# Optimization experiments

Hardware: AMD Instinct MI355X
Metric: run time of the kernel (lower is better)

The kernel has to match this reference:

```python
import jax, jax.numpy as jnp
import numpy as np

N_NODES = 100000
N_EDGES = 1600000
IN_F = 64
HID_F = 64
HID_CH = 32
OUT_F = 16


def setup_inputs() -> dict:
    key = jax.random.key(0)
    ks = jax.random.split(key, 12)
    feat = jax.random.normal(ks[0], (N_NODES, IN_F), dtype=jnp.float32)
    edge_src = jax.random.randint(ks[1], (N_EDGES,), 0, N_NODES, dtype=jnp.int32)
    edge_dst = jax.random.randint(ks[2], (N_EDGES,), 0, N_NODES, dtype=jnp.int32)
    s = 1.414 / np.sqrt(IN_F)
    fc1_w = jax.random.normal(ks[3], (HID_F, IN_F), dtype=jnp.float32) * s
    fc1_b = jnp.zeros((HID_F,), dtype=jnp.float32)
    filt_w = jax.random.normal(ks[4], (HID_F, IN_F), dtype=jnp.float32) * s
    filt_b = jnp.zeros((HID_F,), dtype=jnp.float32)
    att_w1 = jax.random.normal(ks[5], (HID_F, HID_CH), dtype=jnp.float32) * (1.0 / np.sqrt(HID_F))
    att_b1 = jnp.zeros((HID_CH,), dtype=jnp.float32)
    att_w2 = jax.random.normal(ks[6], (HID_CH, 1), dtype=jnp.float32) * (1.0 / np.sqrt(HID_CH))
    fc2_w = jax.random.normal(ks[7], (OUT_F, HID_F), dtype=jnp.float32) * (1.414 / np.sqrt(HID_F))
    fc2_b = jnp.zeros((OUT_F,), dtype=jnp.float32)
    return {
        "feat": feat, "edge_src": edge_src, "edge_dst": edge_dst,
        "fc1_w": fc1_w, "fc1_b": fc1_b, "filt_w": filt_w, "filt_b": filt_b,
        "att_w1": att_w1, "att_b1": att_b1, "att_w2": att_w2,
        "fc2_w": fc2_w, "fc2_b": fc2_b,
    }


def _lp_filter(feat, edge_src, edge_dst, filt_w, filt_b):
    # Low-pass (GCN-style) filter: symmetric-normalized neighborhood aggregation
    # of the linearly transformed features.  x: [N, H]
    x = feat @ filt_w.T + filt_b
    ones = jnp.ones((edge_src.shape[0],), dtype=x.dtype)
    deg_out = jax.ops.segment_sum(ones, edge_src, num_segments=N_NODES)
    deg_in = jax.ops.segment_sum(ones, edge_dst, num_segments=N_NODES)
    inv_sqrt_out = jax.lax.rsqrt(jnp.maximum(deg_out, 1.0))
    inv_sqrt_in = jax.lax.rsqrt(jnp.maximum(deg_in, 1.0))
    # gather-transform-scatter: msg_e = x[src_e] * norm_e  ->  sum at dst
    coef = inv_sqrt_out[edge_src] * inv_sqrt_in[edge_dst]  # [E]
    msg = x[edge_src] * coef[:, None]                       # [E, H]
    return jax.ops.segment_sum(msg, edge_dst, num_segments=N_NODES)  # [N, H]


def _channel_attention(z, att_w1, att_b1, att_w2):
    # z: [N, C, H]; semantic (channel) attention a la HAN
    w = jnp.tanh(z @ att_w1 + att_b1) @ att_w2        # [N, C, 1]
    beta = jax.nn.softmax(w.mean(axis=0), axis=0)     # [C, 1]
    return (beta[None, :, :] * z).sum(axis=1)         # [N, H]


def reference(feat, edge_src, edge_dst, fc1_w, fc1_b, filt_w, filt_b,
              att_w1, att_b1, att_w2, fc2_w, fc2_b):
    h1 = jnp.tanh(feat @ fc1_w.T + fc1_b)                          # MLP branch [N, H]
    h2 = _lp_filter(feat, edge_src, edge_dst, filt_w, filt_b)      # graph branch [N, H]
    z = jnp.stack([h1, h2], axis=1)                                # [N, 2, H]
    fused = _channel_attention(z, att_w1, att_b1, att_w2)          # [N, H]
    return fused @ fc2_w.T + fc2_b                                 # [N, OUT_F]
```

## Files before the change

### kernel.cpp

```cpp
#include <hip/hip_runtime.h>
#include <math.h>

#define N_NODESC 100000
#define N_EDGESC 1600000
#define NBUCK 1563
#define BSLACK 1280
#define SCHUNK 4096
#define NSBLK 391

__device__ __forceinline__ float fast_tanh(float x) {
    float ax = fabsf(x);
    float e = __expf(-2.f * ax);
    float r = (1.f - e) * __builtin_amdgcn_rcpf(1.f + e);
    return copysignf(r, x);
}

__global__ void binit_kernel(int* __restrict__ bcur, int* __restrict__ sbcur) {
    int i = blockIdx.x * blockDim.x + threadIdx.x;
    if (i < NBUCK) { bcur[i] = i * BSLACK; sbcur[i] = i * BSLACK; }
}

__global__ __launch_bounds__(1024) void scatter_dual_kernel(
    const int* __restrict__ src, const int* __restrict__ dst,
    int* __restrict__ bcur, int* __restrict__ sbcur,
    unsigned* __restrict__ bedges, unsigned char* __restrict__ sbytes) {
    __shared__ int histd[NBUCK];
    __shared__ int hists[NBUCK];
    int tid = threadIdx.x;
    int e_beg = blockIdx.x * SCHUNK;
    int e_end = min(e_beg + SCHUNK, N_EDGESC);
    for (int i = tid; i < NBUCK; i += 1024) { histd[i] = 0; hists[i] = 0; }
    __syncthreads();

    int ss[4], dd[4];
    int cnt = 0;
    for (int i = e_beg + tid; i < e_end; i += 1024) {
        ss[cnt] = src[i];
        dd[cnt] = dst[i];
        cnt++;
    }
#pragma unroll
    for (int j = 0; j < 4; j++) {
        if (j < cnt) {
            atomicAdd(&histd[dd[j] >> 6], 1);
            atomicAdd(&hists[ss[j] >> 6], 1);
        }
    }
    __syncthreads();
    for (int i = tid; i < NBUCK; i += 1024) {
        int c = histd[i];
        if (c > 0) histd[i] = atomicAdd(&bcur[i], c);
        int c2 = hists[i];
        if (c2 > 0) hists[i] = atomicAdd(&sbcur[i], c2);
    }
    __syncthreads();
#pragma unroll
    for (int j = 0; j < 4; j++) {
        if (j < cnt) {
            int slot = atomicAdd(&histd[dd[j] >> 6], 1);
            bedges[slot] = (unsigned)ss[j] | ((unsigned)(dd[j] & 63) << 17);
            int slot2 = atomicAdd(&hists[ss[j] >> 6], 1);
            sbytes[slot2] = (unsigned char)(ss[j] & 63);
        }
    }
}

__global__ __launch_bounds__(256) void gemm_kernel(
    const float* __restrict__ feat,
    const float* __restrict__ w1, const float* __restrict__ b1,
    const float* __restrict__ w2, const float* __restrict__ b2,
    const int* __restrict__ sbcur, const unsigned char* __restrict__ sbytes,
    float* __restrict__ h1, float* __restrict__ xs) {
    __shared__ float sf[128 * 68];
    __shared__ int ldeg[128];
    int tid = threadIdx.x;
    int base = blockIdx.x * 128;
    if (tid < 128) ldeg[tid] = 0;
    for (int k = 0; k < 8; k++) {
        int fi = tid + k * 256;
        int node = fi >> 4, f4 = fi & 15;
        float4 v = make_float4(0.f, 0.f, 0.f, 0.f);
        if (base + node < N_NODESC)
            v = ((const float4*)feat)[(size_t)(base + node) * 16 + f4];
        float* d = &sf[node * 68 + f4 * 4];
        d[0] = v.x; d[1] = v.y; d[2] = v.z; d[3] = v.w;
    }
    __syncthreads();

#pragma unroll
    for (int h = 0; h < 2; h++) {
        int sb = blockIdx.x * 2 + h;
        if (sb < NBUCK) {
            int sbeg = sb * BSLACK;
            int sm = sbcur[sb] - sbeg;
            for (int i = tid; i < sm; i += 256)
                atomicAdd(&ldeg[h * 64 + (int)sbytes[sbeg + i]], 1);
        }
    }

    int lane = tid & 63;
    int og = __builtin_amdgcn_readfirstlane(tid >> 6);
    const float* wp1 = w1 + og * 16 * 64;
    const float* wp2 = w2 + og * 16 * 64;

    float a1[2][16], a2[2][16];
#pragma unroll
    for (int o = 0; o < 16; o++) {
        float bb1 = b1[og * 16 + o], bb2 = b2[og * 16 + o];
        a1[0][o] = bb1; a1[1][o] = bb1;
        a2[0][o] = bb2; a2[1][o] = bb2;
    }

    for (int fq = 0; fq < 16; fq++) {
        float4 fv0 = *(const float4*)&sf[lane * 68 + fq * 4];
        float4 fv1 = *(const float4*)&sf[(lane + 64) * 68 + fq * 4];
#pragma unroll
        for (int o = 0; o < 16; o++) {
            float4 wv1 = *(const float4*)&wp1[o * 64 + fq * 4];
            float4 wv2 = *(const float4*)&wp2[o * 64 + fq * 4];
            a1[0][o] += fv0.x * wv1.x + fv0.y * wv1.y + fv0.z * wv1.z + fv0.w * wv1.w;
            a1[1][o] += fv1.x * wv1.x + fv1.y * wv1.y + fv1.z * wv1.z + fv1.w * wv1.w;
            a2[0][o] += fv0.x * wv2.x + fv0.y * wv2.y + fv0.z * wv2.z + fv0.w * wv2.w;
            a2[1][o] += fv1.x * wv2.x + fv1.y * wv2.y + fv1.z * wv2.z + fv1.w * wv2.w;
        }
    }

    __syncthreads();

#pragma unroll
    for (int j = 0; j < 2; j++) {
        int g = base + lane + j * 64;
        if (g >= N_NODESC) continue;
        float is = rsqrtf(fmaxf((float)ldeg[j * 64 + lane], 1.f));
#pragma unroll
        for (int oq = 0; oq < 4; oq++) {
            float4 t, u;
            t.x = fast_tanh(a1[j][oq * 4 + 0]); t.y = fast_tanh(a1[j][oq * 4 + 1]);
            t.z = fast_tanh(a1[j][oq * 4 + 2]); t.w = fast_tanh(a1[j][oq * 4 + 3]);
            u.x = a2[j][oq * 4 + 0] * is;   u.y = a2[j][oq * 4 + 1] * is;
            u.z = a2[j][oq * 4 + 2] * is;   u.w = a2[j][oq * 4 + 3] * is;
            ((float4*)h1)[(size_t)g * 16 + og * 4 + oq] = t;
            ((float4*)xs)[(size_t)g * 16 + og * 4 + oq] = u;
        }
    }
}

__global__ __launch_bounds__(256) void agg4_kernel(const int* __restrict__ bcur,
                                                   const unsigned* __restrict__ bedges,
                                                   const float* __restrict__ xs,
                                                   float* __restrict__ h2) {
    __shared__ unsigned eraw[BSLACK];
    __shared__ unsigned eled[BSLACK];
    __shared__ int loff[65];
    __shared__ int lcnt[64];
    __shared__ int lcur[64];
    int tid = threadIdx.x, lane = tid & 63, wid = tid >> 6;
    int b = blockIdx.x;
    int beg = b * BSLACK;
    int m = bcur[b] - beg;

    if (tid < 64) lcnt[tid] = 0;
    __syncthreads();
    for (int i = tid; i < m; i += 256) {
        unsigned pk = bedges[beg + i];
        eraw[i] = pk;
        atomicAdd(&lcnt[pk >> 17], 1);
    }
    __syncthreads();
    if (wid == 0) {
        int c = lcnt[lane];
        int v = c;
#pragma unroll
        for (int off = 1; off < 64; off <<= 1) {
            int t = __shfl_up(v, off, 64);
            if (lane >= off) v += t;
        }
        loff[lane] = v - c;
        lcur[lane] = v - c;
        if (lane == 63) loff[64] = v;
    }
    __syncthreads();
    for (int i = tid; i < m; i += 256) {
        unsigned pk = eraw[i];
        int pos = atomicAdd(&lcur[pk >> 17], 1);
        eled[pos] = pk & 0x1FFFFu;
    }
    __syncthreads();

    int nbase = b * 64;
#pragma unroll 1
    for (int t = 0; t < 16; t++) {
        int nl = wid * 16 + t;
        int s0 = loff[nl], s1 = loff[nl + 1];
        float acc = 0.f;
        for (int k = s0; k < s1; k += 16) {
            int cnt = s1 - k; if (cnt > 16) cnt = 16;
            unsigned sv = eled[min(k + (lane & 15), s1 - 1)];
            float v[16];
#pragma unroll
            for (int j = 0; j < 16; j++) {
                if (j < cnt) {
                    int sj = __shfl((int)sv, j, 64);
                    v[j] = xs[(size_t)sj * 64 + lane];
                }
            }
#pragma unroll
            for (int j = 0; j < 16; j++)
                if (j < cnt) acc += v[j];
        }
        int g = nbase + nl;
        if (g < N_NODESC) {
            float isq = rsqrtf(fmaxf((float)(s1 - s0), 1.f));
            h2[(size_t)g * 64 + lane] = acc * isq;
        }
    }
}

__global__ __launch_bounds__(256) void att_kernel(const float* __restrict__ h1,
                                                  const float* __restrict__ h2,
                                                  const float* __restrict__ aw1,
                                                  const float* __restrict__ ab1,
                                                  const float* __restrict__ aw2,
                                                  float* __restrict__ wsum) {
    __shared__ float sw1[64 * 32];
    __shared__ float sb1[32];
    __shared__ float sw2[32];
    int tid = threadIdx.x;
    for (int i = tid; i < 64 * 32; i += 256) sw1[i] = aw1[i];
    if (tid < 32) { sb1[tid] = ab1[tid]; sw2[tid] = aw2[tid]; }
    __syncthreads();

    int n = blockIdx.x * 256 + tid;
    float sc[2] = {0.f, 0.f};
    if (n < N_NODESC) {
#pragma unroll
        for (int c = 0; c < 2; c++) {
            const float* row = (c == 0 ? h1 : h2) + (size_t)n * 64;
            float acc[32];
#pragma unroll
            for (int k = 0; k < 32; k++) acc[k] = sb1[k];
            for (int fq = 0; fq < 16; fq++) {
                float4 rv = ((const float4*)row)[fq];
#pragma unroll
                for (int k = 0; k < 32; k++) {
                    acc[k] += rv.x * sw1[(fq * 4 + 0) * 32 + k]
                            + rv.y * sw1[(fq * 4 + 1) * 32 + k]
                            + rv.z * sw1[(fq * 4 + 2) * 32 + k]
                            + rv.w * sw1[(fq * 4 + 3) * 32 + k];
                }
            }
            float s = 0.f;
#pragma unroll
            for (int k = 0; k < 32; k++) s += fast_tanh(acc[k]) * sw2[k];
            sc[c] = s;
        }
    }
#pragma unroll
    for (int off = 32; off; off >>= 1) {
        sc[0] += __shfl_down(sc[0], off, 64);
        sc[1] += __shfl_down(sc[1], off, 64);
    }
    if ((threadIdx.x & 63) == 0) {
        atomicAdd(&wsum[0], sc[0]);
        atomicAdd(&wsum[1], sc[1]);
    }
}

__global__ void beta_kernel(const float* __restrict__ wsum, float* __restrict__ beta) {
    float w0 = wsum[0] / (float)N_NODESC, w1 = wsum[1] / (float)N_NODESC;
    float m = fmaxf(w0, w1);
    float e0 = expf(w0 - m), e1 = expf(w1 - m);
    float inv = 1.f / (e0 + e1);
    beta[0] = e0 * inv;
    beta[1] = e1 * inv;
}

__global__ __launch_bounds__(256) void out_kernel(const float* __restrict__ h1,
                                                  const float* __restrict__ h2,
                                                  const float* __restrict__ beta,
                                                  const float* __restrict__ w,
                                                  const float* __restrict__ b,
                                                  float* __restrict__ out) {
    __shared__ float sw[16 * 68];
    int tid = threadIdx.x;
    {
        int o = tid >> 4, f4 = tid & 15;
        float4 v = ((const float4*)w)[tid];
        float* d = &sw[o * 68 + f4 * 4];
        d[0] = v.x; d[1] = v.y; d[2] = v.z; d[3] = v.w;
    }
    __syncthreads();
    int o = tid & 15, ln = tid >> 4;
    int node = blockIdx.x * 16 + ln;
    if (node >= N_NODESC) return;
    float b0 = beta[0], b1v = beta[1];
    const float4* r1 = (const float4*)(h1 + (size_t)node * 64);
    const float4* r2 = (const float4*)(h2 + (size_t)node * 64);
    float acc = b[o];
    for (int fq = 0; fq < 16; fq++) {
        float4 x1 = r1[fq], x2 = r2[fq];
        float4 wv = *(const float4*)&sw[o * 68 + fq * 4];
        acc += (b0 * x1.x + b1v * x2.x) * wv.x + (b0 * x1.y + b1v * x2.y) * wv.y
             + (b0 * x1.z + b1v * x2.z) * wv.z + (b0 * x1.w + b1v * x2.w) * wv.w;
    }
    out[(size_t)node * 16 + o] = acc;
}

extern "C" void kernel_launch(void* const* d_in, const int* in_sizes, int n_in,
                              void* d_out, int out_size, void* d_ws, size_t ws_size,
                              hipStream_t stream) {
    (void)in_sizes; (void)n_in; (void)out_size; (void)ws_size;
    const float* feat = (const float*)d_in[0];
    const int*   esrc = (const int*)d_in[1];
    const int*   edst = (const int*)d_in[2];
    const float* fc1w = (const float*)d_in[3];
    const float* fc1b = (const float*)d_in[4];
    const float* fltw = (const float*)d_in[5];
    const float* fltb = (const float*)d_in[6];
    const float* aw1  = (const float*)d_in[7];
    const float* ab1  = (const float*)d_in[8];
    const float* aw2  = (const float*)d_in[9];
    const float* fc2w = (const float*)d_in[10];
    const float* fc2b = (const float*)d_in[11];
    float* out = (float*)d_out;

    char* ws = (char*)d_ws;
    size_t off = 0;
    auto alloc = [&](size_t bytes) {
        char* p = ws + off;
        off += (bytes + 255) & ~(size_t)255;
        return p;
    };
    float*         h1     = (float*)alloc((size_t)N_NODESC * 64 * 4);
    float*         xs     = (float*)alloc((size_t)N_NODESC * 64 * 4);
    float*         h2     = (float*)alloc((size_t)N_NODESC * 64 * 4);
    int*           bcur   = (int*)alloc((size_t)NBUCK * 4);
    int*           sbcur  = (int*)alloc((size_t)NBUCK * 4);
    unsigned*      bedges = (unsigned*)alloc((size_t)NBUCK * BSLACK * 4);
    unsigned char* sbytes = (unsigned char*)alloc((size_t)NBUCK * BSLACK);
    float*         wsum   = (float*)alloc(16 * 4);
    float*         beta   = (float*)alloc(16 * 4);

    hipMemsetAsync(wsum, 0, 2 * 4, stream);

    binit_kernel<<<(NBUCK + 255) / 256, 256, 0, stream>>>(bcur, sbcur);
    scatter_dual_kernel<<<NSBLK, 1024, 0, stream>>>(esrc, edst, bcur, sbcur,
                                                    bedges, sbytes);
    gemm_kernel<<<(N_NODESC + 127) / 128, 256, 0, stream>>>(
        feat, fc1w, fc1b, fltw, fltb, sbcur, sbytes, h1, xs);
    agg4_kernel<<<NBUCK, 256, 0, stream>>>(bcur, bedges, xs, h2);
    att_kernel<<<(N_NODESC + 255) / 256, 256, 0, stream>>>(h1, h2, aw1, ab1, aw2, wsum);
    beta_kernel<<<1, 1, 0, stream>>>(wsum, beta);
    out_kernel<<<(N_NODESC + 15) / 16, 256, 0, stream>>>(h1, h2, beta, fc2w, fc2b, out);
}
```

Baseline: 322.4 us.

## Restructure attention scoring to stage node tiles in LDS and split outputs across waves

Measured after the change: 318.3 us. No clear change (-1.3%).

```diff
diff --git a/kernel.cpp b/kernel.cpp
--- a/kernel.cpp
+++ b/kernel.cpp
@@ -216,54 +216,70 @@
     }
 }
 
-__global__ __launch_bounds__(256) void att_kernel(const float* __restrict__ h1,
-                                                  const float* __restrict__ h2,
-                                                  const float* __restrict__ aw1,
-                                                  const float* __restrict__ ab1,
-                                                  const float* __restrict__ aw2,
-                                                  float* __restrict__ wsum) {
-    __shared__ float sw1[64 * 32];
-    __shared__ float sb1[32];
-    __shared__ float sw2[32];
+__global__ __launch_bounds__(256) void att2_kernel(const float* __restrict__ h1,
+                                                   const float* __restrict__ h2,
+                                                   const float* __restrict__ aw1,
+                                                   const float* __restrict__ ab1,
+                                                   const float* __restrict__ aw2,
+                                                   float* __restrict__ wsum) {
+    __shared__ float sf[128 * 68];
+    __shared__ float ssc[2][4][128];
     int tid = threadIdx.x;
-    for (int i = tid; i < 64 * 32; i += 256) sw1[i] = aw1[i];
-    if (tid < 32) { sb1[tid] = ab1[tid]; sw2[tid] = aw2[tid]; }
-    __syncthreads();
-
-    int n = blockIdx.x * 256 + tid;
-    float sc[2] = {0.f, 0.f};
-    if (n < N_NODESC) {
-#pragma unroll
-        for (int c = 0; c < 2; c++) {
-            const float* row = (c == 0 ? h1 : h2) + (size_t)n * 64;
-            float acc[32];
-#pragma unroll
-            for (int k = 0; k < 32; k++) acc[k] = sb1[k];
-            for (int fq = 0; fq < 16; fq++) {
-                float4 rv = ((const float4*)row)[fq];
-#pragma unroll
-                for (int k = 0; k < 32; k++) {
-                    acc[k] += rv.x * sw1[(fq * 4 + 0) * 32 + k]
-                            + rv.y * sw1[(fq * 4 + 1) * 32 + k]
-                            + rv.z * sw1[(fq * 4 + 2) * 32 + k]
-                            + rv.w * sw1[(fq * 4 + 3) * 32 + k];
-                }
+    int lane = tid & 63;
+    int og = __builtin_amdgcn_readfirstlane(tid >> 6);
+    int base = blockIdx.x * 128;
+
+#pragma unroll
+    for (int ch = 0; ch < 2; ch++) {
+        const float* H = ch ? h2 : h1;
+        for (int k = 0; k < 8; k++) {
+            int fi = tid + k * 256;
+            int node = fi >> 4, f4 = fi & 15;
+            float4 v = make_float4(0.f, 0.f, 0.f, 0.f);
+            if (base + node < N_NODESC)
+                v = ((const float4*)H)[(size_t)(base + node) * 16 + f4];
+            float* d = &sf[node * 68 + f4 * 4];
+            d[0] = v.x; d[1] = v.y; d[2] = v.z; d[3] = v.w;
+        }
+        __syncthreads();
+
+        float acc[2][8];
+#pragma unroll
+        for (int c = 0; c < 8; c++) {
+            float bb = ab1[og * 8 + c];
+            acc[0][c] = bb; acc[1][c] = bb;
+        }
+        for (int fq = 0; fq < 16; fq++) {
+            float4 fv0 = *(const float4*)&sf[lane * 68 + fq * 4];
+            float4 fv1 = *(const float4*)&sf[(lane + 64) * 68 + fq * 4];
+#pragma unroll
+            for (int c = 0; c < 8; c++) {
+                float w0 = aw1[(fq * 4 + 0) * 32 + og * 8 + c];
+                float w1 = aw1[(fq * 4 + 1) * 32 + og * 8 + c];
+                float w2 = aw1[(fq * 4 + 2) * 32 + og * 8 + c];
+                float w3 = aw1[(fq * 4 + 3) * 32 + og * 8 + c];
+                acc[0][c] += fv0.x * w0 + fv0.y * w1 + fv0.z * w2 + fv0.w * w3;
+                acc[1][c] += fv1.x * w0 + fv1.y * w1 + fv1.z * w2 + fv1.w * w3;
             }
-            float s = 0.f;
-#pragma unroll
-            for (int k = 0; k < 32; k++) s += fast_tanh(acc[k]) * sw2[k];
-            sc[c] = s;
-        }
-    }
-#pragma unroll
-    for (int off = 32; off; off >>= 1) {
-        sc[0] += __shfl_down(sc[0], off, 64);
-        sc[1] += __shfl_down(sc[1], off, 64);
-    }
-    if ((threadIdx.x & 63) == 0) {
-        atomicAdd(&wsum[0], sc[0]);
-        atomicAdd(&wsum[1], sc[1]);
-    }
+        }
+        float s0 = 0.f, s1 = 0.f;
+#pragma unroll
+        for (int c = 0; c < 8; c++) {
+            float w2c = aw2[og * 8 + c];
+            s0 += fast_tanh(acc[0][c]) * w2c;
+            s1 += fast_tanh(acc[1][c]) * w2c;
+        }
+        ssc[ch][og][lane] = s0;
+        ssc[ch][og][lane + 64] = s1;
+        __syncthreads();
+    }
+
+    int ch = tid >> 7, node = tid & 127;
+    float v = ssc[ch][0][node] + ssc[ch][1][node] + ssc[ch][2][node] + ssc[ch][3][node];
+    if (base + node >= N_NODESC) v = 0.f;
+#pragma unroll
+    for (int off = 32; off; off >>= 1) v += __shfl_down(v, off, 64);
+    if (lane == 0) atomicAdd(&wsum[ch], v);
 }
 
 __global__ void beta_kernel(const float* __restrict__ wsum, float* __restrict__ beta) {
@@ -349,7 +365,7 @@
     gemm_kernel<<<(N_NODESC + 127) / 128, 256, 0, stream>>>(
         feat, fc1w, fc1b, fltw, fltb, sbcur, sbytes, h1, xs);
     agg4_kernel<<<NBUCK, 256, 0, stream>>>(bcur, bedges, xs, h2);
-    att_kernel<<<(N_NODESC + 255) / 256, 256, 0, stream>>>(h1, h2, aw1, ab1, aw2, wsum);
+    att2_kernel<<<(N_NODESC + 127) / 128, 256, 0, stream>>>(h1, h2, aw1, ab1, aw2, wsum);
     beta_kernel<<<1, 1, 0, stream>>>(wsum, beta);
     out_kernel<<<(N_NODESC + 15) / 16, 256, 0, stream>>>(h1, h2, beta, fc2w, fc2b, out);
 }
```
